# Optimization experiments

Hardware: AMD Instinct MI355X
Metric: run time of the kernel (lower is better)

Reference implementation:

```python
import jax, jax.numpy as jnp
import numpy as np
from jax import lax

IN_CH = 192
CENTER_CH = 192
MID_CH = 192
K = 3
BS, H, W = 8, 64, 64
MASK_NUM = 16


def conv2d(x, w, b, padding=0, groups=1):
    # x: (N,C,H,W), w: (O, I/groups, kh, kw)
    out = lax.conv_general_dilated(
        x, w, window_strides=(1, 1),
        padding=[(padding, padding), (padding, padding)],
        dimension_numbers=('NCHW', 'OIHW', 'NCHW'),
        feature_group_count=groups)
    return out + b[None, :, None, None]


def lrelu(x):
    return jax.nn.leaky_relu(x, negative_slope=0.1)


def setup_inputs() -> dict:
    key = jax.random.key(0)
    ks = jax.random.split(key, 32)
    s = 0.02
    d = {
        'input': jax.random.normal(ks[0], (BS, IN_CH, H, W), jnp.float32),
        'list_center': jax.random.normal(ks[1], (BS, MASK_NUM, CENTER_CH), jnp.float32),
        'batch_mask': jax.random.randint(ks[2], (BS, H, W), 0, MASK_NUM),
        # self.conv: conv1x1(in,mid) -> lrelu -> conv1x1(mid,mid)
        'w0': jax.random.normal(ks[3], (MID_CH, IN_CH, 1, 1)) * s,
        'b0': jnp.zeros((MID_CH,)),
        'w1': jax.random.normal(ks[4], (MID_CH, MID_CH, 1, 1)) * s,
        'b1': jnp.zeros((MID_CH,)),
        # k_sp_gen: conv1x1(mid+center,mid), 3x3(mid,mid), depthwise 3x3(mid -> mid*k^2, groups=mid)
        'ws0': jax.random.normal(ks[5], (MID_CH, MID_CH + CENTER_CH, 1, 1)) * s,
        'bs0': jnp.zeros((MID_CH,)),
        'ws1': jax.random.normal(ks[6], (MID_CH, MID_CH, K, K)) * s,
        'bs1': jnp.zeros((MID_CH,)),
        'ws2': jax.random.normal(ks[7], (MID_CH * K * K, 1, K, K)) * s,
        'bs2': jnp.zeros((MID_CH * K * K,)),
        # k_ch_gen: GAP -> conv1x1 -> lrelu -> conv1x1 -> sigmoid
        'wc0': jax.random.normal(ks[8], (MID_CH, MID_CH, 1, 1)) * s,
        'bc0': jnp.zeros((MID_CH,)),
        'wc1': jax.random.normal(ks[9], (MID_CH, MID_CH, 1, 1)) * s,
        'bc1': jnp.zeros((MID_CH,)),
        # conv_out
        'wo': jax.random.normal(ks[10], (IN_CH, MID_CH, 1, 1)) * s,
        'bo': jnp.zeros((IN_CH,)),
    }
    return d


def mask_expand(list_center, batch_mask):
    # list_center: (bs, mask_num, ch); batch_mask: (bs, h, w) int
    # -> (bs, ch, h, w)
    gathered = jax.vmap(lambda c, m: c[m])(list_center, batch_mask)  # (bs,h,w,ch)
    return jnp.transpose(gathered, (0, 3, 1, 2))


def dynamic_conv(x, k_sp, k):
    # x: (bs, ch, h, w); k_sp: (bs, ch, k^2, h, w)
    bs, ch, h, w = x.shape
    p = (k - 1) // 2
    xp = jnp.pad(x, ((0, 0), (0, 0), (p, p), (p, p)))
    # torch Unfold ordering: kernel index = ki*k + kj, channel-major in view
    patches = jnp.stack([xp[:, :, i:i + h, j:j + w]
                         for i in range(k) for j in range(k)], axis=2)
    return jnp.einsum('bckhw,bckhw->bchw', patches, k_sp)


def reference(input, list_center, batch_mask, w0, b0, w1, b1, ws0, bs0,
              ws1, bs1, ws2, bs2, wc0, bc0, wc1, bc1, wo, bo):
    bs, _, h, w = input.shape
    k = K
    ch = MID_CH
    centers_exp = mask_expand(list_center, batch_mask)  # (bs, center_ch, h, w)
    shortcut = input
    x = conv2d(lrelu(conv2d(input, w0, b0)), w1, b1)  # self.conv
    y = jnp.concatenate([x, centers_exp], axis=1)
    y = lrelu(conv2d(y, ws0, bs0))
    y = lrelu(conv2d(y, ws1, bs1, padding=(k - 1) // 2))
    k_sp = conv2d(y, ws2, bs2, padding=(k - 1) // 2, groups=ch)
    k_sp = k_sp.reshape(bs, ch, k * k, h, w)
    out = dynamic_conv(x, k_sp, k)
    # squeeze-excite channel gate
    g = jnp.mean(out, axis=(2, 3), keepdims=True)
    g = jax.nn.sigmoid(conv2d(lrelu(conv2d(g, wc0, bc0)), wc1, bc1))
    out = g * out
    out = conv2d(out, wo, bo)
    return out + shortcut
```

## Files before the change

kernel.cpp:

```cpp
#include <hip/hip_runtime.h>
#include <hip/hip_bf16.h>

#define CH   192
#define PIX  4096
#define BSZ  8

using f32x4  = __attribute__((ext_vector_type(4))) float;
using short8 = __attribute__((ext_vector_type(8))) short;

__device__ __forceinline__ float bf2f(unsigned short u) {
    union { unsigned u32; float f; } x; x.u32 = ((unsigned)u) << 16; return x.f;
}
__device__ __forceinline__ unsigned short f2bf(float f) {
    union { float f; unsigned u; } x; x.f = f;
    unsigned u = x.u;
    unsigned r = (u + 0x7FFFu + ((u >> 16) & 1u)) >> 16;
    return (unsigned short)r;
}

__global__ void k_prep_w(const float* __restrict__ w0, const float* __restrict__ w1,
                         const float* __restrict__ ws0, const float* __restrict__ wo,
                         const float* __restrict__ ws1, const float* __restrict__ lc,
                         const float* __restrict__ wc0, const float* __restrict__ wc1,
                         unsigned short* __restrict__ w0f, unsigned short* __restrict__ w1f,
                         unsigned short* __restrict__ ws0xf, unsigned short* __restrict__ wof,
                         unsigned short* __restrict__ wc3f, float* __restrict__ tc,
                         float* __restrict__ wc0t, float* __restrict__ wc1t) {
    int i = blockIdx.x * 256 + threadIdx.x;
    if (i < 4*36864) {
        int which = i / 36864, j = i % 36864;
        int kc = j / 6144, r = j % 6144, mf = r / 512, r2 = r % 512;
        int l = r2 >> 3, e = r2 & 7;
        int o = mf*16 + (l & 15), k = kc*32 + ((l >> 4) << 3) + e;
        float v;
        unsigned short* dst;
        if (which == 0)      { v = w0[o*192 + k];  dst = w0f;   }
        else if (which == 1) { v = w1[o*192 + k];  dst = w1f;   }
        else if (which == 2) { v = ws0[o*384 + k]; dst = ws0xf; }
        else                 { v = wo[o*192 + k];  dst = wof;   }
        dst[j] = f2bf(v);
        return;
    }
    i -= 4*36864;
    if (i < 331776) {
        int tk = i / 6144, tap = tk / 6, kc = tk % 6;
        int r = i % 6144, mf = r / 512, r2 = r % 512;
        int l = r2 >> 3, e = r2 & 7;
        int o = mf*16 + (l & 15), c = kc*32 + ((l >> 4) << 3) + e;
        wc3f[i] = f2bf(ws1[(o*192 + c)*9 + tap]);
        return;
    }
    i -= 331776;
    if (i < 24576) {
        int bm = i / 192, o = i % 192;
        const float* wr = ws0 + o*384 + 192;
        const float* cb = lc + bm*192;
        float a = 0.f;
        for (int c2 = 0; c2 < 192; ++c2) a += wr[c2] * cb[c2];
        tc[i] = a;
        return;
    }
    i -= 24576;
    if (i < 36864) { int o = i / 192, c = i % 192; wc0t[c*192 + o] = wc0[o*192 + c]; return; }
    i -= 36864;
    if (i < 36864) { int o = i / 192, c = i % 192; wc1t[c*192 + o] = wc1[o*192 + c]; }
}

__global__ __launch_bounds__(256) void k_fused3(
    const float* __restrict__ input,
    const unsigned short* __restrict__ w0f,
    const unsigned short* __restrict__ w1f,
    const unsigned short* __restrict__ ws0xf,
    const float* __restrict__ b0, const float* __restrict__ b1,
    const float* __restrict__ bs0,
    const float* __restrict__ tc, const int* __restrict__ mask,
    unsigned short* __restrict__ xg, unsigned short* __restrict__ y0t)
{
    const int b = blockIdx.y, n0 = blockIdx.x * 64;
    __shared__ unsigned short Bsm[64*200];
    __shared__ unsigned short Csm[64*200];
    const int tid = threadIdx.x, lane = tid & 63, wv = tid >> 6;
    const int li = lane & 15, kq = lane >> 4;

    {
        const float* src = input + (size_t)b*192*PIX + n0;
        #pragma unroll
        for (int j = 0; j < 6; ++j) {
            int q = tid + 256*j, k = q >> 3, g = (q & 7)*8;
            float4 v0 = *(const float4*)(src + (size_t)k*PIX + g);
            float4 v1 = *(const float4*)(src + (size_t)k*PIX + g + 4);
            Bsm[(g+0)*200 + k] = f2bf(v0.x);
            Bsm[(g+1)*200 + k] = f2bf(v0.y);
            Bsm[(g+2)*200 + k] = f2bf(v0.z);
            Bsm[(g+3)*200 + k] = f2bf(v0.w);
            Bsm[(g+4)*200 + k] = f2bf(v1.x);
            Bsm[(g+5)*200 + k] = f2bf(v1.y);
            Bsm[(g+6)*200 + k] = f2bf(v1.z);
            Bsm[(g+7)*200 + k] = f2bf(v1.w);
        }
    }
    __syncthreads();

    f32x4 acc[3][4];

    #pragma unroll
    for (int m = 0; m < 3; ++m)
        #pragma unroll
        for (int n = 0; n < 4; ++n) acc[m][n] = {0.f,0.f,0.f,0.f};
    for (int kc = 0; kc < 6; ++kc) {
        short8 a[3];
        #pragma unroll
        for (int m = 0; m < 3; ++m)
            a[m] = *(const short8*)(w0f + ((kc*12 + wv*3 + m)*64 + lane)*8);
        #pragma unroll
        for (int n = 0; n < 4; ++n) {
            short8 fb = *(const short8*)(Bsm + (n*16 + li)*200 + kc*32 + kq*8);
            #pragma unroll
            for (int m = 0; m < 3; ++m)
                acc[m][n] = __builtin_amdgcn_mfma_f32_16x16x32_bf16(a[m], fb, acc[m][n], 0,0,0);
        }
    }
    #pragma unroll
    for (int m = 0; m < 3; ++m) {
        int o0 = (wv*3 + m)*16 + kq*4;
        #pragma unroll
        for (int n = 0; n < 4; ++n) {
            int px = n*16 + li;
            ushort4 w;
            unsigned short* wp = (unsigned short*)&w;
            #pragma unroll
            for (int r = 0; r < 4; ++r) {
                float v = acc[m][n][r] + b0[o0 + r];
                v = v > 0.f ? v : 0.1f*v;
                wp[r] = f2bf(v);
            }
            *(ushort4*)(Csm + px*200 + o0) = w;
        }
    }
    __syncthreads();

    #pragma unroll
    for (int m = 0; m < 3; ++m)
        #pragma unroll
        for (int n = 0; n < 4; ++n) acc[m][n] = {0.f,0.f,0.f,0.f};
    for (int kc = 0; kc < 6; ++kc) {
        short8 a[3];
        #pragma unroll
        for (int m = 0; m < 3; ++m)
            a[m] = *(const short8*)(w1f + ((kc*12 + wv*3 + m)*64 + lane)*8);
        #pragma unroll
        for (int n = 0; n < 4; ++n) {
            short8 fb = *(const short8*)(Csm + (n*16 + li)*200 + kc*32 + kq*8);
            #pragma unroll
            for (int m = 0; m < 3; ++m)
                acc[m][n] = __builtin_amdgcn_mfma_f32_16x16x32_bf16(a[m], fb, acc[m][n], 0,0,0);
        }
    }
    #pragma unroll
    for (int m = 0; m < 3; ++m) {
        int o0 = (wv*3 + m)*16 + kq*4;
        #pragma unroll
        for (int n = 0; n < 4; ++n) {
            int px = n*16 + li;
            ushort4 w;
            unsigned short* wp = (unsigned short*)&w;
            #pragma unroll
            for (int r = 0; r < 4; ++r) {
                float v = acc[m][n][r] + b1[o0 + r];
                unsigned short h = f2bf(v);
                wp[r] = h;
                xg[((size_t)b*192 + o0 + r)*PIX + n0 + px] = h;
            }
            *(ushort4*)(Bsm + px*200 + o0) = w;
        }
    }
    __syncthreads();

    #pragma unroll
    for (int m = 0; m < 3; ++m)
        #pragma unroll
        for (int n = 0; n < 4; ++n) acc[m][n] = {0.f,0.f,0.f,0.f};
    for (int kc = 0; kc < 6; ++kc) {
        short8 a[3];
        #pragma unroll
        for (int m = 0; m < 3; ++m)
            a[m] = *(const short8*)(ws0xf + ((kc*12 + wv*3 + m)*64 + lane)*8);
        #pragma unroll
        for (int n = 0; n < 4; ++n) {
            short8 fb = *(const short8*)(Bsm + (n*16 + li)*200 + kc*32 + kq*8);
            #pragma unroll
            for (int m = 0; m < 3; ++m)
                acc[m][n] = __builtin_amdgcn_mfma_f32_16x16x32_bf16(a[m], fb, acc[m][n], 0,0,0);
        }
    }
    int mi_[4];
    #pragma unroll
    for (int n = 0; n < 4; ++n) mi_[n] = mask[b*PIX + n0 + n*16 + li];
    #pragma unroll
    for (int m = 0; m < 3; ++m) {
        int o0 = (wv*3 + m)*16 + kq*4;
        #pragma unroll
        for (int n = 0; n < 4; ++n) {
            int px = n*16 + li;
            const float* tcb = tc + (b*16 + mi_[n])*192;
            ushort4 w;
            unsigned short* wp = (unsigned short*)&w;
            #pragma unroll
            for (int r = 0; r < 4; ++r) {
                float v = acc[m][n][r] + bs0[o0 + r] + tcb[o0 + r];
                v = v > 0.f ? v : 0.1f*v;
                wp[r] = f2bf(v);
            }
            *(ushort4*)(Csm + px*200 + o0) = w;
        }
    }
    __syncthreads();
    #pragma unroll
    for (int j = 0; j < 6; ++j) {
        int u = tid + 256*j;
        int px = u / 24, chunk = u % 24;
        uint4 v = *(const uint4*)(Csm + px*200 + chunk*8);
        *(uint4*)(y0t + ((size_t)(b*4096 + n0 + px))*192 + chunk*8) = v;
    }
}

__global__ __launch_bounds__(512) void k_conv3t(
    const unsigned short* __restrict__ wc3f,
    const unsigned short* __restrict__ y0t,
    const float* __restrict__ bias,
    unsigned short* __restrict__ y1)
{
    const int b = blockIdx.y, h = blockIdx.x;
    __shared__ unsigned short Bs[2][3*66*40];
    const int tid = threadIdx.x, lane = tid & 63, wv = tid >> 6;
    const int li = lane & 15, kq = lane >> 4;
    const int mw = wv >> 1, nh = wv & 1;

    const int u1 = tid + 512;
    const int r0 = tid >> 2,  c0 = tid & 3;
    const int dr0 = r0/66, px0g = r0%66 - 1, hh0 = h + dr0 - 1;
    const bool ok0 = ((unsigned)hh0 < 64u) & ((unsigned)px0g < 64u);
    const size_t s0 = ok0 ? ((size_t)(b*4096 + hh0*64 + px0g))*192 + c0*8 : 0;
    const int o0f = r0*80 + c0*16;
    const int r1 = u1 >> 2,  c1 = u1 & 3;
    const int dr1 = r1/66, px1g = r1%66 - 1, hh1 = h + dr1 - 1;
    const bool act1 = (u1 < 792);
    const bool ok1 = act1 & ((unsigned)hh1 < 64u) & ((unsigned)px1g < 64u);
    const size_t s1 = ok1 ? ((size_t)(b*4096 + hh1*64 + px1g))*192 + c1*8 : 0;
    const int o1f = r1*80 + c1*16;
    const uint4 zz = {0u,0u,0u,0u};

    uint4 v0, v1;
    v0 = ok0 ? *(const uint4*)(y0t + s0) : zz;
    v1 = ok1 ? *(const uint4*)(y0t + s1) : zz;
    *(uint4*)((char*)Bs[0] + o0f) = v0;
    if (act1) *(uint4*)((char*)Bs[0] + o1f) = v1;
    __syncthreads();

    f32x4 acc[3][2];
    #pragma unroll
    for (int m = 0; m < 3; ++m)
        #pragma unroll
        for (int nn = 0; nn < 2; ++nn) acc[m][nn] = {0.f,0.f,0.f,0.f};

    for (int kc = 0; kc < 6; ++kc) {
        const int cur = kc & 1;
        if (kc < 5) {
            v0 = ok0 ? *(const uint4*)(y0t + s0 + (kc+1)*32) : zz;
            v1 = ok1 ? *(const uint4*)(y0t + s1 + (kc+1)*32) : zz;
        }
        const unsigned short* Bc = Bs[cur];
        #pragma unroll
        for (int tap = 0; tap < 9; ++tap) {
            const int dr = tap / 3, dc1 = tap % 3;
            short8 a[3];
            #pragma unroll
            for (int m = 0; m < 3; ++m)
                a[m] = *(const short8*)(wc3f + (((tap*6 + kc)*12 + mw*3 + m)*64 + lane)*8);
            #pragma unroll
            for (int nn = 0; nn < 2; ++nn) {
                int pxi = nh*32 + nn*16 + li + dc1;
                short8 fb = *(const short8*)((const char*)Bc + (dr*66 + pxi)*80 + kq*16);
                #pragma unroll
                for (int m = 0; m < 3; ++m)
                    acc[m][nn] = __builtin_amdgcn_mfma_f32_16x16x32_bf16(a[m], fb, acc[m][nn], 0,0,0);
            }
        }
        if (kc < 5) {
            *(uint4*)((char*)Bs[cur^1] + o0f) = v0;
            if (act1) *(uint4*)((char*)Bs[cur^1] + o1f) = v1;
            __syncthreads();
        }
    }

    #pragma unroll
    for (int m = 0; m < 3; ++m) {
        int oo = (mw*3 + m)*16 + kq*4;
        #pragma unroll
        for (int nn = 0; nn < 2; ++nn) {
            int px = h*64 + nh*32 + nn*16 + li;
            #pragma unroll
            for (int r = 0; r < 4; ++r) {
                float v = acc[m][nn][r] + bias[oo + r];
                v = v > 0.f ? v : 0.1f*v;
                y1[((size_t)b*192 + oo + r)*PIX + px] = f2bf(v);
            }
        }
    }
}

__global__ __launch_bounds__(256) void k_dwdyn3(
    const unsigned short* __restrict__ Y1,
    const unsigned short* __restrict__ X,
    const float* __restrict__ ws2,
    const float* __restrict__ bs2,
    unsigned short* __restrict__ OP,
    float* __restrict__ gsum)
{
    const int c = blockIdx.x, b = blockIdx.y;
    __shared__ unsigned short ysm[4096];
    __shared__ unsigned short xsm[4096];
    __shared__ float red[4];
    const int tid = threadIdx.x;
    const size_t cb = ((size_t)b*192 + c) * PIX;
    #pragma unroll
    for (int j = 0; j < 2; ++j) {
        int i = tid + 256*j;
        *(uint4*)(ysm + i*8) = *(const uint4*)(Y1 + cb + i*8);
        *(uint4*)(xsm + i*8) = *(const uint4*)(X  + cb + i*8);
    }
    float wreg[81], breg[9];
    #pragma unroll
    for (int t = 0; t < 81; ++t) wreg[t] = ws2[c*81 + t];
    #pragma unroll
    for (int t = 0; t < 9; ++t) breg[t] = bs2[c*9 + t];
    __syncthreads();

    const int w = tid & 63, rg = tid >> 6, h0 = rg * 16;
    const bool wl = (w > 0), wr = (w < 63);

    float ya[3], yb[3], yc[3], xa[3], xb[3], xc[3];
    {
        int h = h0 - 1;
        if (h >= 0) {
            int base = h*64 + w;
            ya[0] = wl ? bf2f(ysm[base-1]) : 0.f;  ya[1] = bf2f(ysm[base]);
            ya[2] = wr ? bf2f(ysm[base+1]) : 0.f;
            xa[0] = wl ? bf2f(xsm[base-1]) : 0.f;  xa[1] = bf2f(xsm[base]);
            xa[2] = wr ? bf2f(xsm[base+1]) : 0.f;
        } else { ya[0]=ya[1]=ya[2]=0.f; xa[0]=xa[1]=xa[2]=0.f; }
        int base = h0*64 + w;
        yb[0] = wl ? bf2f(ysm[base-1]) : 0.f;  yb[1] = bf2f(ysm[base]);
        yb[2] = wr ? bf2f(ysm[base+1]) : 0.f;
        xb[0] = wl ? bf2f(xsm[base-1]) : 0.f;  xb[1] = bf2f(xsm[base]);
        xb[2] = wr ? bf2f(xsm[base+1]) : 0.f;
    }

    float gacc = 0.f;
    #pragma unroll 4
    for (int j = 0; j < 16; ++j) {
        int h = h0 + j;
        if (h + 1 < 64) {
            int base = (h+1)*64 + w;
            yc[0] = wl ? bf2f(ysm[base-1]) : 0.f;  yc[1] = bf2f(ysm[base]);
            yc[2] = wr ? bf2f(ysm[base+1]) : 0.f;
            xc[0] = wl ? bf2f(xsm[base-1]) : 0.f;  xc[1] = bf2f(xsm[base]);
            xc[2] = wr ? bf2f(xsm[base+1]) : 0.f;
        } else { yc[0]=yc[1]=yc[2]=0.f; xc[0]=xc[1]=xc[2]=0.f; }

        float ksp[9];
        #pragma unroll
        for (int t = 0; t < 9; ++t) ksp[t] = breg[t];
        #pragma unroll
        for (int tj = 0; tj < 3; ++tj) {
            #pragma unroll
            for (int t = 0; t < 9; ++t) ksp[t] += ya[tj] * wreg[t*9 + tj];
            #pragma unroll
            for (int t = 0; t < 9; ++t) ksp[t] += yb[tj] * wreg[t*9 + 3 + tj];
            #pragma unroll
            for (int t = 0; t < 9; ++t) ksp[t] += yc[tj] * wreg[t*9 + 6 + tj];
        }
        float out = xa[0]*ksp[0] + xa[1]*ksp[1] + xa[2]*ksp[2]
                  + xb[0]*ksp[3] + xb[1]*ksp[4] + xb[2]*ksp[5]
                  + xc[0]*ksp[6] + xc[1]*ksp[7] + xc[2]*ksp[8];
        OP[cb + h*64 + w] = f2bf(out);
        gacc += out;
        #pragma unroll
        for (int t = 0; t < 3; ++t) {
            ya[t] = yb[t]; yb[t] = yc[t];
            xa[t] = xb[t]; xb[t] = xc[t];
        }
    }
    #pragma unroll
    for (int off = 32; off > 0; off >>= 1) gacc += __shfl_down(gacc, off);
    if ((tid & 63) == 0) red[tid >> 6] = gacc;
    __syncthreads();
    if (tid == 0) gsum[b*192 + c] = red[0] + red[1] + red[2] + red[3];
}

__global__ __launch_bounds__(256) void k_gemmo(
    const unsigned short* __restrict__ wof,
    const unsigned short* __restrict__ op,
    const float* __restrict__ bo,
    const float* __restrict__ gsum,
    const float* __restrict__ wc0t, const float* __restrict__ bc0,
    const float* __restrict__ wc1t, const float* __restrict__ bc1,
    const float* __restrict__ resid,
    float* __restrict__ out)
{
    const int b = blockIdx.y, n0 = blockIdx.x * 64;
    __shared__ unsigned short Bsm[64*200];
    __shared__ float mean[192], s1[192], gv[192];
    const int tid = threadIdx.x, lane = tid & 63, wv = tid >> 6;
    const int li = lane & 15, kq = lane >> 4;

    if (tid < 192) mean[tid] = gsum[b*192 + tid] * (1.f/4096.f);
    __syncthreads();
    if (tid < 192) {
        float a = bc0[tid];
        for (int i = 0; i < 192; ++i) a += wc0t[i*192 + tid] * mean[i];
        s1[tid] = a > 0.f ? a : 0.1f * a;
    }
    __syncthreads();
    if (tid < 192) {
        float a2 = bc1[tid];
        for (int i = 0; i < 192; ++i) a2 += wc1t[i*192 + tid] * s1[i];
        gv[tid] = 1.f / (1.f + __expf(-a2));
    }
    __syncthreads();

    {
        const unsigned short* src = op + (size_t)b*192*PIX + n0;
        #pragma unroll
        for (int j = 0; j < 6; ++j) {
            int q = tid + 256*j, c = q >> 3, g = (q & 7) * 8;
            uint4 v = *(const uint4*)(src + (size_t)c*PIX + g);
            float gs = gv[c];
            const unsigned short* pv = (const unsigned short*)&v;
            #pragma unroll
            for (int e = 0; e < 8; ++e)
                Bsm[(g+e)*200 + c] = f2bf(bf2f(pv[e]) * gs);
        }
    }
    __syncthreads();

    f32x4 acc[3][4];
    #pragma unroll
    for (int m = 0; m < 3; ++m)
        #pragma unroll
        for (int n = 0; n < 4; ++n) acc[m][n] = {0.f,0.f,0.f,0.f};
    for (int kc = 0; kc < 6; ++kc) {
        short8 a[3];
        #pragma unroll
        for (int m = 0; m < 3; ++m)
            a[m] = *(const short8*)(wof + ((kc*12 + wv*3 + m)*64 + lane)*8);
        #pragma unroll
        for (int n = 0; n < 4; ++n) {
            short8 fb = *(const short8*)(Bsm + (n*16 + li)*200 + kc*32 + kq*8);
            #pragma unroll
            for (int m = 0; m < 3; ++m)
                acc[m][n] = __builtin_amdgcn_mfma_f32_16x16x32_bf16(a[m], fb, acc[m][n], 0,0,0);
        }
    }
    #pragma unroll
    for (int m = 0; m < 3; ++m) {
        int o0 = (wv*3 + m)*16 + kq*4;
        #pragma unroll
        for (int n = 0; n < 4; ++n) {
            int px = n*16 + li;
            #pragma unroll
            for (int r = 0; r < 4; ++r) {
                size_t idx = ((size_t)b*192 + o0 + r)*PIX + n0 + px;
                out[idx] = acc[m][n][r] + bo[o0 + r] + resid[idx];
            }
        }
    }
}

extern "C" void kernel_launch(void* const* d_in, const int* in_sizes, int n_in,
                              void* d_out, int out_size, void* d_ws, size_t ws_size,
                              hipStream_t stream)
{
    const float* input = (const float*)d_in[0];
    const float* lc    = (const float*)d_in[1];
    const int*   mask  = (const int*)d_in[2];
    const float* w0  = (const float*)d_in[3];
    const float* b0  = (const float*)d_in[4];
    const float* w1  = (const float*)d_in[5];
    const float* b1  = (const float*)d_in[6];
    const float* ws0 = (const float*)d_in[7];
    const float* bs0 = (const float*)d_in[8];
    const float* ws1 = (const float*)d_in[9];
    const float* bs1 = (const float*)d_in[10];
    const float* ws2 = (const float*)d_in[11];
    const float* bs2 = (const float*)d_in[12];
    const float* wc0 = (const float*)d_in[13];
    const float* bc0 = (const float*)d_in[14];
    const float* wc1 = (const float*)d_in[15];
    const float* bc1 = (const float*)d_in[16];
    const float* wo  = (const float*)d_in[17];
    const float* bo  = (const float*)d_in[18];

    char* ws = (char*)d_ws;
    size_t off = 0;
    auto alloc = [&](size_t bytes) {
        void* p = ws + off; off = (off + bytes + 255) & ~(size_t)255; return p;
    };
    const size_t act_b = (size_t)BSZ * CH * PIX * 2;
    unsigned short* x_bf  = (unsigned short*)alloc(act_b);
    unsigned short* y0t   = (unsigned short*)alloc(act_b);
    unsigned short* y1_bf = (unsigned short*)alloc(act_b);
    unsigned short* op_bf = (unsigned short*)alloc(act_b);
    unsigned short* w0f   = (unsigned short*)alloc(36864*2);
    unsigned short* w1f   = (unsigned short*)alloc(36864*2);
    unsigned short* ws0xf = (unsigned short*)alloc(36864*2);
    unsigned short* wof   = (unsigned short*)alloc(36864*2);
    unsigned short* wc3f  = (unsigned short*)alloc(331776*2);
    float* tc    = (float*)alloc(8*16*192*4);
    float* gsum  = (float*)alloc(1536*4);
    float* wc0t  = (float*)alloc(36864*4);
    float* wc1t  = (float*)alloc(36864*4);

    k_prep_w<<<2256, 256, 0, stream>>>(w0, w1, ws0, wo, ws1, lc, wc0, wc1,
                                       w0f, w1f, ws0xf, wof, wc3f, tc, wc0t, wc1t);

    dim3 gg(64, 8);
    k_fused3<<<gg, 256, 0, stream>>>(input, w0f, w1f, ws0xf, b0, b1, bs0, tc, mask, x_bf, y0t);
    k_conv3t<<<gg, 512, 0, stream>>>(wc3f, y0t, bs1, y1_bf);
    k_dwdyn3<<<dim3(192, 8), 256, 0, stream>>>(y1_bf, x_bf, ws2, bs2, op_bf, gsum);
    k_gemmo<<<gg, 256, 0, stream>>>(wof, op_bf, bo, gsum, wc0t, bc0, wc1t, bc1,
                                    input, (float*)d_out);
}
```

Baseline: 218.8 us.

## Process two output rows per 3x3 conv block and move depthwise weights to LDS

The 3x3 conv kernel now computes two image rows per block, staging a 4-row halo instead of 3 and keeping 12 accumulator tiles per wave. This amortizes the weight-fragment loads and the halo traffic across twice as many output pixels. It also halves the grid to 256 blocks, which may leave CUs underused and raise register pressure. Separately, the depthwise dynamic kernel reads its 81 weights and 9 biases from shared memory instead of per-thread registers, trading register pressure for LDS reads.

Result: no change. 221.9 us (+1.4%).

```diff
diff --git a/kernel.cpp b/kernel.cpp
--- a/kernel.cpp
+++ b/kernel.cpp
@@ -224,50 +224,50 @@
     }
 }
 
-__global__ __launch_bounds__(512) void k_conv3t(
+__global__ __launch_bounds__(512) void k_conv3w(
     const unsigned short* __restrict__ wc3f,
     const unsigned short* __restrict__ y0t,
     const float* __restrict__ bias,
     unsigned short* __restrict__ y1)
 {
-    const int b = blockIdx.y, h = blockIdx.x;
-    __shared__ unsigned short Bs[2][3*66*40];
+    const int b = blockIdx.y, h0 = blockIdx.x * 2;
+    __shared__ unsigned short Bs[2][4*66*40];
     const int tid = threadIdx.x, lane = tid & 63, wv = tid >> 6;
     const int li = lane & 15, kq = lane >> 4;
     const int mw = wv >> 1, nh = wv & 1;
 
-    const int u1 = tid + 512;
-    const int r0 = tid >> 2,  c0 = tid & 3;
-    const int dr0 = r0/66, px0g = r0%66 - 1, hh0 = h + dr0 - 1;
-    const bool ok0 = ((unsigned)hh0 < 64u) & ((unsigned)px0g < 64u);
-    const size_t s0 = ok0 ? ((size_t)(b*4096 + hh0*64 + px0g))*192 + c0*8 : 0;
-    const int o0f = r0*80 + c0*16;
-    const int r1 = u1 >> 2,  c1 = u1 & 3;
-    const int dr1 = r1/66, px1g = r1%66 - 1, hh1 = h + dr1 - 1;
-    const bool act1 = (u1 < 792);
-    const bool ok1 = act1 & ((unsigned)hh1 < 64u) & ((unsigned)px1g < 64u);
-    const size_t s1 = ok1 ? ((size_t)(b*4096 + hh1*64 + px1g))*192 + c1*8 : 0;
-    const int o1f = r1*80 + c1*16;
+    size_t src[3]; int dstf[3]; bool ok[3], act[3];
+    #pragma unroll
+    for (int s = 0; s < 3; ++s) {
+        int u = tid + 512*s;
+        act[s] = (u < 1056);
+        int row = u >> 2, chunk = u & 3;
+        int r = row / 66, pxl = row % 66;
+        int hh = h0 + r - 1, pxg = pxl - 1;
+        ok[s] = act[s] & ((unsigned)hh < 64u) & ((unsigned)pxg < 64u);
+        src[s] = ok[s] ? ((size_t)(b*4096 + hh*64 + pxg))*192 + chunk*8 : 0;
+        dstf[s] = row*80 + chunk*16;
+    }
     const uint4 zz = {0u,0u,0u,0u};
-
-    uint4 v0, v1;
-    v0 = ok0 ? *(const uint4*)(y0t + s0) : zz;
-    v1 = ok1 ? *(const uint4*)(y0t + s1) : zz;
-    *(uint4*)((char*)Bs[0] + o0f) = v0;
-    if (act1) *(uint4*)((char*)Bs[0] + o1f) = v1;
-    __syncthreads();
-
-    f32x4 acc[3][2];
+    uint4 v[3];
+    #pragma unroll
+    for (int s = 0; s < 3; ++s) v[s] = ok[s] ? *(const uint4*)(y0t + src[s]) : zz;
+    #pragma unroll
+    for (int s = 0; s < 3; ++s) if (act[s]) *(uint4*)((char*)Bs[0] + dstf[s]) = v[s];
+    __syncthreads();
+
+    f32x4 acc[3][4];
     #pragma unroll
     for (int m = 0; m < 3; ++m)
         #pragma unroll
-        for (int nn = 0; nn < 2; ++nn) acc[m][nn] = {0.f,0.f,0.f,0.f};
+        for (int n = 0; n < 4; ++n) acc[m][n] = {0.f,0.f,0.f,0.f};
 
     for (int kc = 0; kc < 6; ++kc) {
         const int cur = kc & 1;
         if (kc < 5) {
-            v0 = ok0 ? *(const uint4*)(y0t + s0 + (kc+1)*32) : zz;
-            v1 = ok1 ? *(const uint4*)(y0t + s1 + (kc+1)*32) : zz;
+            #pragma unroll
+            for (int s = 0; s < 3; ++s)
+                v[s] = ok[s] ? *(const uint4*)(y0t + src[s] + (kc+1)*32) : zz;
         }
         const unsigned short* Bc = Bs[cur];
         #pragma unroll
@@ -277,18 +277,20 @@
             #pragma unroll
             for (int m = 0; m < 3; ++m)
                 a[m] = *(const short8*)(wc3f + (((tap*6 + kc)*12 + mw*3 + m)*64 + lane)*8);
-            #pragma unroll
-            for (int nn = 0; nn < 2; ++nn) {
-                int pxi = nh*32 + nn*16 + li + dc1;
-                short8 fb = *(const short8*)((const char*)Bc + (dr*66 + pxi)*80 + kq*16);
+            const int rowi = nh + dr;
+            #pragma unroll
+            for (int n = 0; n < 4; ++n) {
+                int pxi = n*16 + li + dc1;
+                short8 fb = *(const short8*)((const char*)Bc + (rowi*66 + pxi)*80 + kq*16);
                 #pragma unroll
                 for (int m = 0; m < 3; ++m)
-                    acc[m][nn] = __builtin_amdgcn_mfma_f32_16x16x32_bf16(a[m], fb, acc[m][nn], 0,0,0);
+                    acc[m][n] = __builtin_amdgcn_mfma_f32_16x16x32_bf16(a[m], fb, acc[m][n], 0,0,0);
             }
         }
         if (kc < 5) {
-            *(uint4*)((char*)Bs[cur^1] + o0f) = v0;
-            if (act1) *(uint4*)((char*)Bs[cur^1] + o1f) = v1;
+            #pragma unroll
+            for (int s = 0; s < 3; ++s)
+                if (act[s]) *(uint4*)((char*)Bs[cur^1] + dstf[s]) = v[s];
             __syncthreads();
         }
     }
@@ -297,13 +299,13 @@
     for (int m = 0; m < 3; ++m) {
         int oo = (mw*3 + m)*16 + kq*4;
         #pragma unroll
-        for (int nn = 0; nn < 2; ++nn) {
-            int px = h*64 + nh*32 + nn*16 + li;
+        for (int n = 0; n < 4; ++n) {
+            int px = (h0 + nh)*64 + n*16 + li;
             #pragma unroll
             for (int r = 0; r < 4; ++r) {
-                float v = acc[m][nn][r] + bias[oo + r];
-                v = v > 0.f ? v : 0.1f*v;
-                y1[((size_t)b*192 + oo + r)*PIX + px] = f2bf(v);
+                float vv = acc[m][n][r] + bias[oo + r];
+                vv = vv > 0.f ? vv : 0.1f*vv;
+                y1[((size_t)b*192 + oo + r)*PIX + px] = f2bf(vv);
             }
         }
     }
@@ -320,7 +322,7 @@
     const int c = blockIdx.x, b = blockIdx.y;
     __shared__ unsigned short ysm[4096];
     __shared__ unsigned short xsm[4096];
-    __shared__ float red[4];
+    __shared__ float wsm[81], bsm9[9], red[4];
     const int tid = threadIdx.x;
     const size_t cb = ((size_t)b*192 + c) * PIX;
     #pragma unroll
@@ -329,11 +331,8 @@
         *(uint4*)(ysm + i*8) = *(const uint4*)(Y1 + cb + i*8);
         *(uint4*)(xsm + i*8) = *(const uint4*)(X  + cb + i*8);
     }
-    float wreg[81], breg[9];
-    #pragma unroll
-    for (int t = 0; t < 81; ++t) wreg[t] = ws2[c*81 + t];
-    #pragma unroll
-    for (int t = 0; t < 9; ++t) breg[t] = bs2[c*9 + t];
+    if (tid < 81) wsm[tid] = ws2[c*81 + tid];
+    else if (tid < 90) bsm9[tid-81] = bs2[c*9 + tid - 81];
     __syncthreads();
 
     const int w = tid & 63, rg = tid >> 6, h0 = rg * 16;
@@ -370,15 +369,15 @@
 
         float ksp[9];
         #pragma unroll
-        for (int t = 0; t < 9; ++t) ksp[t] = breg[t];
+        for (int t = 0; t < 9; ++t) ksp[t] = bsm9[t];
         #pragma unroll
         for (int tj = 0; tj < 3; ++tj) {
             #pragma unroll
-            for (int t = 0; t < 9; ++t) ksp[t] += ya[tj] * wreg[t*9 + tj];
-            #pragma unroll
-            for (int t = 0; t < 9; ++t) ksp[t] += yb[tj] * wreg[t*9 + 3 + tj];
-            #pragma unroll
-            for (int t = 0; t < 9; ++t) ksp[t] += yc[tj] * wreg[t*9 + 6 + tj];
+            for (int t = 0; t < 9; ++t) ksp[t] += ya[tj] * wsm[t*9 + tj];
+            #pragma unroll
+            for (int t = 0; t < 9; ++t) ksp[t] += yb[tj] * wsm[t*9 + 3 + tj];
+            #pragma unroll
+            for (int t = 0; t < 9; ++t) ksp[t] += yc[tj] * wsm[t*9 + 6 + tj];
         }
         float out = xa[0]*ksp[0] + xa[1]*ksp[1] + xa[2]*ksp[2]
                   + xb[0]*ksp[3] + xb[1]*ksp[4] + xb[2]*ksp[5]
@@ -526,7 +525,7 @@
 
     dim3 gg(64, 8);
     k_fused3<<<gg, 256, 0, stream>>>(input, w0f, w1f, ws0xf, b0, b1, bs0, tc, mask, x_bf, y0t);
-    k_conv3t<<<gg, 512, 0, stream>>>(wc3f, y0t, bs1, y1_bf);
+    k_conv3w<<<dim3(32, 8), 512, 0, stream>>>(wc3f, y0t, bs1, y1_bf);
     k_dwdyn3<<<dim3(192, 8), 256, 0, stream>>>(y1_bf, x_bf, ws2, bs2, op_bf, gsum);
     k_gemmo<<<gg, 256, 0, stream>>>(wof, op_bf, bo, gsum, wc0t, bc0, wc1t, bc1,
                                     input, (float*)d_out);
```
